# Optimization experiments

Measured on AMD Instinct MI355X. Metric: run time of the kernel, lower is better.

The kernel has to match this reference:

```python
import jax, jax.numpy as jnp
import numpy as np

D_MODEL = 1024
N_HEADS = 16
D_K = D_MODEL // N_HEADS
THETA = 10000.0
NEG_INF = -1e30


def _rope_tables(token_positions, d_k, theta=THETA):
    # freqs[t, i] = t / theta**(2i/d_k), i in [0, d_k/2)
    exponent = jnp.arange(0, d_k, 2, dtype=jnp.float32)  # [d_k/2]
    inv_freq = 1.0 / theta ** (exponent / d_k)
    freqs = token_positions.astype(jnp.float32)[:, None] * inv_freq[None, :]  # [s, d_k/2]
    return jnp.cos(freqs), jnp.sin(freqs)


def _apply_rope(x, cos, sin):
    # x: [..., s, d_k]; interleaved pair rotation (pairs are (x[2i], x[2i+1]))
    x1 = x[..., 0::2]
    x2 = x[..., 1::2]
    r1 = x1 * cos - x2 * sin
    r2 = x1 * sin + x2 * cos
    return jnp.stack([r1, r2], axis=-1).reshape(x.shape)


def setup_inputs() -> dict:
    key = jax.random.key(0)
    ks = jax.random.split(key, 5)
    b, s = 2, 2048
    scale = np.sqrt(2.0 / (D_MODEL + D_MODEL))
    return {
        "x": jax.random.normal(ks[0], (b, s, D_MODEL), dtype=jnp.float32),
        "Wq": jax.random.normal(ks[1], (D_MODEL, D_MODEL), dtype=jnp.float32) * scale,
        "Wk": jax.random.normal(ks[2], (D_MODEL, D_MODEL), dtype=jnp.float32) * scale,
        "Wv": jax.random.normal(ks[3], (D_MODEL, D_MODEL), dtype=jnp.float32) * scale,
        "Wo": jax.random.normal(ks[4], (D_MODEL, D_MODEL), dtype=jnp.float32) * scale,
        "token_positions": jnp.arange(s, dtype=jnp.int64 if jax.config.jax_enable_x64 else jnp.int32),
    }


def reference(x, Wq, Wk, Wv, Wo, token_positions):
    b, s, _ = x.shape
    # QKV projections: weight stored [in, out]
    q = jnp.einsum('bsi,io->bso', x, Wq)
    k = jnp.einsum('bsi,io->bso', x, Wk)
    v = jnp.einsum('bsi,io->bso', x, Wv)
    # split heads: [b, h, s, d_k]
    q = q.reshape(b, s, N_HEADS, D_K).transpose(0, 2, 1, 3)
    k = k.reshape(b, s, N_HEADS, D_K).transpose(0, 2, 1, 3)
    v = v.reshape(b, s, N_HEADS, D_K).transpose(0, 2, 1, 3)
    # RoPE
    cos, sin = _rope_tables(token_positions, D_K)
    q = _apply_rope(q, cos, sin)
    k = _apply_rope(k, cos, sin)
    # causal attention with full materialized scores (faithful to source)
    scores = jnp.einsum('bhid,bhjd->bhij', q, k) / jnp.sqrt(jnp.float32(D_K))
    mask = jnp.tril(jnp.ones((s, s), dtype=bool))
    scores = jnp.where(mask, scores, NEG_INF)
    probs = jax.nn.softmax(scores, axis=-1)
    out = jnp.einsum('bhij,bhjd->bhid', probs, v)
    out = out.transpose(0, 2, 1, 3).reshape(b, s, D_MODEL)
    return jnp.einsum('bsi,io->bso', out, Wo)
```

## Files before the change

kernel.cpp:

```cpp
#include <hip/hip_runtime.h>
#include <hip/hip_bf16.h>
#include <cmath>

#define S_LEN 2048
#define DMODEL 1024
#define NHEADS 16
#define DK 64
#define BATCH 2
#define MTOT (BATCH * S_LEN)

using short8 = __attribute__((ext_vector_type(8))) short;
using floatx4 = __attribute__((ext_vector_type(4))) float;

__device__ __forceinline__ unsigned short f2b(float f) {
    union { float f; unsigned u; } v; v.f = f;
    unsigned r = v.u + 0x7fff + ((v.u >> 16) & 1);
    return (unsigned short)(r >> 16);
}

__device__ __forceinline__ unsigned pack2(float a, float b) {
    float2 t; t.x = a; t.y = b;
    __hip_bfloat162 h = __float22bfloat162_rn(t);
    union { __hip_bfloat162 h; unsigned u; } v; v.h = h;
    return v.u;
}

__device__ __forceinline__ void gload16(const void* g, void* l) {
    __builtin_amdgcn_global_load_lds(
        (const __attribute__((address_space(1))) unsigned int*)g,
        (__attribute__((address_space(3))) unsigned int*)l, 16, 0, 0);
}

#define FENCE() asm volatile("" ::: "memory")

__global__ __launch_bounds__(256) void prep_k(
    const float* __restrict__ x, unsigned short* __restrict__ xb,
    const int* __restrict__ tokpos, float* __restrict__ ct, float* __restrict__ st,
    const float* W0, const float* W1, const float* W2, const float* W3,
    unsigned short* T0, unsigned short* T1, unsigned short* T2, unsigned short* T3) {
    __shared__ float t[64][65];
    const int b = blockIdx.x;
    if (b < 2048) {
        int i = (b * 256 + threadIdx.x) * 8;
        float4 a = *(const float4*)(x + i);
        float4 bb = *(const float4*)(x + i + 4);
        short8 o;
        o[0] = f2b(a.x); o[1] = f2b(a.y); o[2] = f2b(a.z); o[3] = f2b(a.w);
        o[4] = f2b(bb.x); o[5] = f2b(bb.y); o[6] = f2b(bb.z); o[7] = f2b(bb.w);
        *(short8*)(xb + i) = o;
    } else if (b < 2304) {
        int idx = (b - 2048) * 256 + threadIdx.x;
        int si = idx >> 5;
        int ip = idx & 31;
        float pos = (float)tokpos[si];
        float inv_freq = powf(10000.0f, -(float)(2 * ip) / 64.0f);
        float ang = pos * inv_freq;
        ct[idx] = cosf(ang);
        st[idx] = sinf(ang);
    } else {
        int id = b - 2304;
        int z = id >> 8;
        int bx = id & 15, by = (id >> 4) & 15;
        const float* W = z == 0 ? W0 : z == 1 ? W1 : z == 2 ? W2 : W3;
        unsigned short* T = z == 0 ? T0 : z == 1 ? T1 : z == 2 ? T2 : T3;
        const bool perm = (z < 2);
        int n0 = bx * 64, k0 = by * 64;
        int rr = threadIdx.x >> 6, cc = threadIdx.x & 63;
#pragma unroll
        for (int r = 0; r < 16; r++) {
            int row = r * 4 + rr;
            t[row][cc] = W[(size_t)(k0 + row) * DMODEL + n0 + cc];
        }
        __syncthreads();
#pragma unroll
        for (int r = 0; r < 16; r++) {
            int row = r * 4 + rr;
            int drow = perm ? (((row & 1) ? 32 : 0) + (row >> 1)) : row;
            T[(size_t)(n0 + drow) * DMODEL + k0 + cc] = f2b(t[cc][row]);
        }
    }
}

__global__ __launch_bounds__(256) void vtrans_k(const unsigned short* __restrict__ V,
                                                unsigned short* __restrict__ Vt) {
    __shared__ unsigned short t[64][72];
    const int tid = threadIdx.x;
    const int s0 = blockIdx.x * 64, d0 = blockIdx.y * 64;
    const int bb = s0 >> 11;
#pragma unroll
    for (int it = 0; it < 4; it++) {
        int e = (it * 256 + tid) * 4;
        int r = e >> 6, c = e & 63;
        *(ushort4*)&t[r][c] = *(const ushort4*)(V + (size_t)(s0 + r) * DMODEL + d0 + c);
    }
    __syncthreads();
#pragma unroll
    for (int it = 0; it < 4; it++) {
        int e = (it * 256 + tid) * 4;
        int r = e >> 6, c = e & 63;
        ushort4 v;
        v.x = t[c + 0][r]; v.y = t[c + 1][r];
        v.z = t[c + 2][r]; v.w = t[c + 3][r];
        *(ushort4*)(Vt + (size_t)(bb * 1024 + d0 + r) * S_LEN + (s0 & (S_LEN - 1)) + c) = v;
    }
}

__global__ __launch_bounds__(512, 2) void mm_k(
    const unsigned short* __restrict__ A,
    const unsigned short* __restrict__ Bt0, const unsigned short* __restrict__ Bt1,
    const unsigned short* __restrict__ Bt2,
    void* C0, void* C1, void* C2,
    const float* __restrict__ ct, const float* __restrict__ st, int kind) {
    __shared__ __align__(16) unsigned short blob[10 * 8192];

    const int z = blockIdx.z;
    const unsigned short* Bt = z == 0 ? Bt0 : z == 1 ? Bt1 : Bt2;
    void* C = z == 0 ? C0 : z == 1 ? C1 : C2;
    const int mode = (kind == 1) ? 0 : (z == 2 ? 3 : 1);
    const float qscale = (z == 0 && kind == 0) ? 0.18033688011112042f : 1.0f;

    const int tid = threadIdx.x;
    const int w = tid >> 6, lane = tid & 63;
    const int l15 = lane & 15, quad = lane >> 4;
    const int wr = w >> 2, wc = w & 3;
    const int m0 = blockIdx.x * 256, n0 = blockIdx.y * 256;

    const int rbase = (w >> 1) * 16 + l15;
    const int cbase = (w & 1) * 32 + quad * 8;

    floatx4 acc[8][4];
#pragma unroll
    for (int i = 0; i < 8; i++)
#pragma unroll
        for (int j = 0; j < 4; j++) acc[i][j] = (floatx4){0.f, 0.f, 0.f, 0.f};

    auto stage_half = [&](int h) {
        const int ts = h >> 2, part = h & 3;
        const int slot = h % 10;
        const unsigned short* src =
            (part < 2 ? A + (((size_t)(m0 + part * 128 + rbase)) << 10)
                      : Bt + (((size_t)(n0 + (part - 2) * 128 + rbase)) << 10))
            + (size_t)ts * 64 + cbase;
        char* d = (char*)blob + slot * 16384 + w * 1024;
        gload16(src, d);
        gload16(src + (64 << 10), d + 8192);
    };

#pragma unroll
    for (int h = 0; h < 6; ++h) stage_half(h);
    asm volatile("s_waitcnt vmcnt(4)" ::: "memory");
    FENCE(); __builtin_amdgcn_s_barrier(); FENCE();

    short8 af[4][2];
    for (int t = 0; t < 16; ++t) {
        const int sb = (4 * t) % 10;
        int sA = sb + wr;            if (sA >= 10) sA -= 10;
        int sB = sb + 2 + (wc >> 1); if (sB >= 10) sB -= 10;
        const char* LA = (const char*)blob + sA * 16384;
        const char* LB = (const char*)blob + sB * 16384;
#pragma unroll
        for (int q = 0; q < 4; ++q) {
            const int rh = q >> 1, ch = q & 1;
            if (ch == 0) {
#pragma unroll
                for (int ii = 0; ii < 4; ++ii)
#pragma unroll
                    for (int kh = 0; kh < 2; ++kh)
                        af[ii][kh] = *(const short8*)(LA + ((rh * 4 + ii) * 2 + kh) * 1024 + lane * 16);
            }
            short8 bf[2][2];
#pragma unroll
            for (int jj = 0; jj < 2; ++jj)
#pragma unroll
                for (int kh = 0; kh < 2; ++kh)
                    bf[jj][kh] = *(const short8*)(LB + (((wc & 1) * 4 + ch * 2 + jj) * 2 + kh) * 1024 + lane * 16);
            const int h = 4 * t + q + 6;
            if (h < 64) stage_half(h);
            if (q == 3) {
                if (t == 14) asm volatile("s_waitcnt vmcnt(0)" ::: "memory");
                else         asm volatile("s_waitcnt vmcnt(4)" ::: "memory");
            }
            FENCE(); __builtin_amdgcn_s_barrier(); FENCE();
            __builtin_amdgcn_s_setprio(1);
#pragma unroll
            for (int ii = 0; ii < 4; ++ii)
#pragma unroll
                for (int jj = 0; jj < 2; ++jj) {
                    floatx4 a0 = acc[rh * 4 + ii][ch * 2 + jj];
                    a0 = __builtin_amdgcn_mfma_f32_16x16x32_bf16(af[ii][0], bf[jj][0], a0, 0, 0, 0);
                    a0 = __builtin_amdgcn_mfma_f32_16x16x32_bf16(af[ii][1], bf[jj][1], a0, 0, 0, 0);
                    acc[rh * 4 + ii][ch * 2 + jj] = a0;
                }
            __builtin_amdgcn_s_setprio(0);
            FENCE(); __builtin_amdgcn_s_barrier(); FENCE();
        }
    }

#pragma unroll
    for (int i = 0; i < 8; i++) {
        const int rowb = m0 + wr * 128 + i * 16 + quad * 4;
        if (mode == 0) {
            float* Cf = (float*)C;
#pragma unroll
            for (int j = 0; j < 4; j++) {
                int colb = n0 + wc * 64 + j * 16 + l15;
#pragma unroll
                for (int r = 0; r < 4; r++)
                    Cf[(size_t)(rowb + r) * DMODEL + colb] = acc[i][j][r];
            }
        } else if (mode == 1) {
            unsigned short* Cb = (unsigned short*)C;
#pragma unroll
            for (int jh = 0; jh < 2; jh++) {
                int ip = jh * 16 + l15;
                int cole = n0 + wc * 64 + jh * 16 + l15;
#pragma unroll
                for (int r = 0; r < 4; r++) {
                    int row = rowb + r;
                    int si = row & (S_LEN - 1);
                    float c = ct[si * 32 + ip] * qscale;
                    float s = st[si * 32 + ip] * qscale;
                    float e = acc[i][jh][r];
                    float od = acc[i][jh + 2][r];
                    Cb[(size_t)row * DMODEL + cole] = f2b(e * c - od * s);
                    Cb[(size_t)row * DMODEL + cole + 32] = f2b(e * s + od * c);
                }
            }
        } else {
            unsigned short* Cb = (unsigned short*)C;
#pragma unroll
            for (int j = 0; j < 4; j++) {
                int colb = n0 + wc * 64 + j * 16 + l15;
#pragma unroll
                for (int r = 0; r < 4; r++)
                    Cb[(size_t)(rowb + r) * DMODEL + colb] = f2b(acc[i][j][r]);
            }
        }
    }
}

__global__ __launch_bounds__(512) void attn_k(const unsigned short* __restrict__ Q,
                                              const unsigned short* __restrict__ K,
                                              const unsigned short* __restrict__ Vt,
                                              unsigned short* __restrict__ O) {
    __shared__ __align__(16) unsigned short Kblob[2][4096];
    __shared__ __align__(16) unsigned short Vblob[2][4096];
    __shared__ __align__(16) unsigned short Ps[8][16 * 72];

    const int tid = threadIdx.x;
    const int w = tid >> 6, lane = tid & 63;
    const int l15 = lane & 15, quad = lane >> 4;
    const int idx = blockIdx.x;
    const int qt = 15 - (idx >> 5);
    const int bh = idx & 31;
    const int bb = bh >> 4, h = bh & 15;
    const int qbase = qt * 128 + w * 16;
    const int qrow = qbase + l15;

    const size_t qoff = (size_t)(bb * S_LEN + qbase + l15) * DMODEL + h * DK;
    short8 aq0 = *(const short8*)(Q + qoff + quad * 8);
    short8 aq1 = *(const short8*)(Q + qoff + 32 + quad * 8);

    floatx4 o[4];
#pragma unroll
    for (int f = 0; f < 4; f++) o[f] = (floatx4){0.f, 0.f, 0.f, 0.f};
    float mv = -1e30f, lv = 0.f;

    const unsigned short* Kb = K + (size_t)(bb * S_LEN) * DMODEL + h * DK;
    const unsigned short* Vb = Vt + (size_t)(bb * 1024 + h * DK) * S_LEN;
    unsigned short* ps = &Ps[w][0];

    auto stage = [&](int b, int kb) {
#pragma unroll
        for (int it = 0; it < 2; it++) {
            int g = it * 8 + w;
            if (g < 8) {
                const unsigned short* gp =
                    Kb + (size_t)(kb + (g >> 1) * 16 + l15) * DMODEL + (g & 1) * 32 + quad * 8;
                gload16(gp, (char*)&Kblob[b][0] + g * 1024);
            } else {
                int gv = g - 8;
                const unsigned short* gp =
                    Vb + (size_t)((gv >> 1) * 16 + l15) * S_LEN + kb + (gv & 1) * 32 + quad * 8;
                gload16(gp, (char*)&Vblob[b][0] + gv * 1024);
            }
        }
    };

    const int nkt = 2 * qt + 2;
    stage(0, 0);
    for (int kt = 0; kt < nkt; kt++) {
        const int b = kt & 1;
        const int kb = kt * 64;
        __syncthreads();
        if (kt + 1 < nkt) stage(b ^ 1, (kt + 1) * 64);

        const unsigned short* kbb = &Kblob[b][0];
        floatx4 c[4];
#pragma unroll
        for (int g = 0; g < 4; g++) {
            short8 kf0 = *(const short8*)(kbb + (g * 2 + 0) * 512 + lane * 8);
            short8 kf1 = *(const short8*)(kbb + (g * 2 + 1) * 512 + lane * 8);
            floatx4 t = {0.f, 0.f, 0.f, 0.f};
            t = __builtin_amdgcn_mfma_f32_16x16x32_bf16(kf0, aq0, t, 0, 0, 0);
            c[g] = __builtin_amdgcn_mfma_f32_16x16x32_bf16(kf1, aq1, t, 0, 0, 0);
        }

        float sv[16];
        if (kb + 63 <= qbase) {
#pragma unroll
            for (int g = 0; g < 4; g++)
#pragma unroll
                for (int r = 0; r < 4; r++) sv[g * 4 + r] = c[g][r];
        } else {
#pragma unroll
            for (int g = 0; g < 4; g++)
#pragma unroll
                for (int r = 0; r < 4; r++) {
                    int key = kb + g * 16 + quad * 4 + r;
                    sv[g * 4 + r] = (key <= qrow) ? c[g][r] : -1e30f;
                }
        }
        float mx = sv[0];
#pragma unroll
        for (int i = 1; i < 16; i++) mx = fmaxf(mx, sv[i]);
        mx = fmaxf(mx, __shfl_xor(mx, 16));
        mx = fmaxf(mx, __shfl_xor(mx, 32));
        float mnew = fmaxf(mv, mx);
        float alpha = exp2f(mv - mnew);
        mv = mnew;
        float p[16], psum = 0.f;
#pragma unroll
        for (int i = 0; i < 16; i++) {
            p[i] = exp2f(sv[i] - mnew);
            psum += p[i];
        }
        lv = lv * alpha + psum;

#pragma unroll
        for (int g = 0; g < 4; g++) {
            uint2 pk;
            pk.x = pack2(p[g * 4 + 0], p[g * 4 + 1]);
            pk.y = pack2(p[g * 4 + 2], p[g * 4 + 3]);
            *(uint2*)(ps + l15 * 72 + g * 16 + quad * 4) = pk;
        }
#pragma unroll
        for (int f = 0; f < 4; f++) {
            o[f][0] *= alpha; o[f][1] *= alpha;
            o[f][2] *= alpha; o[f][3] *= alpha;
        }
        short8 pf0 = *(const short8*)(ps + l15 * 72 + quad * 8);
        short8 pf1 = *(const short8*)(ps + l15 * 72 + 32 + quad * 8);
        const unsigned short* vbb = &Vblob[b][0];
#pragma unroll
        for (int f = 0; f < 4; f++) {
            short8 vf0 = *(const short8*)(vbb + (f * 2 + 0) * 512 + lane * 8);
            short8 vf1 = *(const short8*)(vbb + (f * 2 + 1) * 512 + lane * 8);
            o[f] = __builtin_amdgcn_mfma_f32_16x16x32_bf16(vf0, pf0, o[f], 0, 0, 0);
            o[f] = __builtin_amdgcn_mfma_f32_16x16x32_bf16(vf1, pf1, o[f], 0, 0, 0);
        }
    }

    lv += __shfl_xor(lv, 16);
    lv += __shfl_xor(lv, 32);
    float inv = 1.0f / lv;
    __syncthreads();
#pragma unroll
    for (int f = 0; f < 4; f++) {
        uint2 pk;
        pk.x = pack2(o[f][0] * inv, o[f][1] * inv);
        pk.y = pack2(o[f][2] * inv, o[f][3] * inv);
        *(uint2*)(ps + l15 * 72 + f * 16 + quad * 4) = pk;
    }
    short8 r0 = *(const short8*)(ps + l15 * 72 + quad * 8);
    short8 r1 = *(const short8*)(ps + l15 * 72 + 32 + quad * 8);
    size_t obase = (size_t)(bb * S_LEN + qbase + l15) * DMODEL + h * DK;
    *(short8*)(O + obase + quad * 8) = r0;
    *(short8*)(O + obase + 32 + quad * 8) = r1;
}

extern "C" void kernel_launch(void* const* d_in, const int* in_sizes, int n_in,
                              void* d_out, int out_size, void* d_ws,
                              size_t ws_size, hipStream_t stream) {
    const float* x = (const float*)d_in[0];
    const float* Wq = (const float*)d_in[1];
    const float* Wk = (const float*)d_in[2];
    const float* Wv = (const float*)d_in[3];
    const float* Wo = (const float*)d_in[4];
    const int* tokpos = (const int*)d_in[5];
    float* out = (float*)d_out;

    const size_t MD = (size_t)MTOT * DMODEL;
    const size_t WD = (size_t)DMODEL * DMODEL;
    unsigned short* xb = (unsigned short*)d_ws;
    unsigned short* Wqt = xb + MD;
    unsigned short* Wkt = Wqt + WD;
    unsigned short* Wvt = Wkt + WD;
    unsigned short* Wot = Wvt + WD;
    unsigned short* Q = Wot + WD;
    unsigned short* K = Q + MD;
    unsigned short* V = K + MD;
    unsigned short* Vt = V + MD;
    float* ct = (float*)(Vt + MD);
    float* st = ct + S_LEN * 32;
    unsigned short* O = V;

    prep_k<<<dim3(3328), dim3(256), 0, stream>>>(x, xb, tokpos, ct, st,
                                                 Wq, Wk, Wv, Wo, Wqt, Wkt, Wvt, Wot);

    mm_k<<<dim3(16, 4, 3), dim3(512), 0, stream>>>(xb, Wqt, Wkt, Wvt,
                                                   (void*)Q, (void*)K, (void*)V, ct, st, 0);
    vtrans_k<<<dim3(64, 16), dim3(256), 0, stream>>>(V, Vt);
    attn_k<<<dim3(512), dim3(512), 0, stream>>>(Q, K, Vt, O);
    mm_k<<<dim3(16, 4, 1), dim3(512), 0, stream>>>(O, Wot, Wot, Wot,
                                                   (void*)out, (void*)out, (void*)out, ct, st, 1);
}
```

Baseline: 214.9 us.

## Triple-buffer K/V staging with explicit waitcnt barriers and skip masked tiles

Replaces the double-buffered K/V staging with a three-slot ring that prefetches two tiles ahead, using explicit vmcnt waits and raw s_barrier instead of __syncthreads. Each wave now loads one K and one V chunk per stage through incrementing pointers, and waves skip the compute for key tiles fully above their causal diagonal. It also adds a lazy rescale that only updates the running max when it actually grows, raises MFMA priority with setprio, sets a min-blocks launch bound, and changes block ordering for part of the grid. Extra LDS for the third buffer may reduce occupancy, and the hand-written wait counts depend on the gload16 instruction count.

```diff
diff --git a/kernel.cpp b/kernel.cpp
--- a/kernel.cpp
+++ b/kernel.cpp
@@ -239,19 +239,19 @@
     }
 }
 
-__global__ __launch_bounds__(512) void attn_k(const unsigned short* __restrict__ Q,
-                                              const unsigned short* __restrict__ K,
-                                              const unsigned short* __restrict__ Vt,
-                                              unsigned short* __restrict__ O) {
-    __shared__ __align__(16) unsigned short Kblob[2][4096];
-    __shared__ __align__(16) unsigned short Vblob[2][4096];
+__global__ __launch_bounds__(512, 4) void attn_k(const unsigned short* __restrict__ Q,
+                                                 const unsigned short* __restrict__ K,
+                                                 const unsigned short* __restrict__ Vt,
+                                                 unsigned short* __restrict__ O) {
+    __shared__ __align__(16) unsigned short Kblob[3][4096];
+    __shared__ __align__(16) unsigned short Vblob[3][4096];
     __shared__ __align__(16) unsigned short Ps[8][16 * 72];
 
     const int tid = threadIdx.x;
     const int w = tid >> 6, lane = tid & 63;
     const int l15 = lane & 15, quad = lane >> 4;
     const int idx = blockIdx.x;
-    const int qt = 15 - (idx >> 5);
+    const int qt = (idx < 256) ? 15 - (idx >> 5) : ((idx - 256) >> 5);
     const int bh = idx & 31;
     const int bb = bh >> 4, h = bh & 15;
     const int qbase = qt * 128 + w * 16;
@@ -270,95 +270,111 @@
     const unsigned short* Vb = Vt + (size_t)(bb * 1024 + h * DK) * S_LEN;
     unsigned short* ps = &Ps[w][0];
 
-    auto stage = [&](int b, int kb) {
-#pragma unroll
-        for (int it = 0; it < 2; it++) {
-            int g = it * 8 + w;
-            if (g < 8) {
-                const unsigned short* gp =
-                    Kb + (size_t)(kb + (g >> 1) * 16 + l15) * DMODEL + (g & 1) * 32 + quad * 8;
-                gload16(gp, (char*)&Kblob[b][0] + g * 1024);
+    const unsigned short* kp = Kb + (size_t)((w >> 1) * 16 + l15) * DMODEL + (w & 1) * 32 + quad * 8;
+    const unsigned short* vp = Vb + (size_t)((w >> 1) * 16 + l15) * S_LEN + (w & 1) * 32 + quad * 8;
+
+    auto stage = [&](int slot) {
+        gload16(kp, (char*)&Kblob[slot][0] + w * 1024);
+        gload16(vp, (char*)&Vblob[slot][0] + w * 1024);
+        kp += 64 * DMODEL;
+        vp += 64;
+    };
+
+    const int nkt = 2 * qt + 2;
+    stage(0); stage(1);
+    asm volatile("s_waitcnt vmcnt(2)" ::: "memory");
+    FENCE(); __builtin_amdgcn_s_barrier(); FENCE();
+
+    int sl = 0, s2 = 2;
+    for (int kt = 0; kt < nkt; kt++) {
+        if (kt + 2 < nkt) stage(s2);
+
+        if (kt * 64 <= qbase + 15) {
+            const int kb = kt * 64;
+            const unsigned short* kbb = &Kblob[sl][0];
+            floatx4 c[4];
+            __builtin_amdgcn_s_setprio(1);
+#pragma unroll
+            for (int g = 0; g < 4; g++) {
+                short8 kf0 = *(const short8*)(kbb + (g * 2 + 0) * 512 + lane * 8);
+                short8 kf1 = *(const short8*)(kbb + (g * 2 + 1) * 512 + lane * 8);
+                floatx4 t = {0.f, 0.f, 0.f, 0.f};
+                t = __builtin_amdgcn_mfma_f32_16x16x32_bf16(kf0, aq0, t, 0, 0, 0);
+                c[g] = __builtin_amdgcn_mfma_f32_16x16x32_bf16(kf1, aq1, t, 0, 0, 0);
+            }
+            __builtin_amdgcn_s_setprio(0);
+
+            float sv[16];
+            if (kb + 63 <= qbase) {
+#pragma unroll
+                for (int g = 0; g < 4; g++)
+#pragma unroll
+                    for (int r = 0; r < 4; r++) sv[g * 4 + r] = c[g][r];
             } else {
-                int gv = g - 8;
-                const unsigned short* gp =
-                    Vb + (size_t)((gv >> 1) * 16 + l15) * S_LEN + kb + (gv & 1) * 32 + quad * 8;
-                gload16(gp, (char*)&Vblob[b][0] + gv * 1024);
-            }
-        }
-    };
-
-    const int nkt = 2 * qt + 2;
-    stage(0, 0);
-    for (int kt = 0; kt < nkt; kt++) {
-        const int b = kt & 1;
-        const int kb = kt * 64;
-        __syncthreads();
-        if (kt + 1 < nkt) stage(b ^ 1, (kt + 1) * 64);
-
-        const unsigned short* kbb = &Kblob[b][0];
-        floatx4 c[4];
-#pragma unroll
-        for (int g = 0; g < 4; g++) {
-            short8 kf0 = *(const short8*)(kbb + (g * 2 + 0) * 512 + lane * 8);
-            short8 kf1 = *(const short8*)(kbb + (g * 2 + 1) * 512 + lane * 8);
-            floatx4 t = {0.f, 0.f, 0.f, 0.f};
-            t = __builtin_amdgcn_mfma_f32_16x16x32_bf16(kf0, aq0, t, 0, 0, 0);
-            c[g] = __builtin_amdgcn_mfma_f32_16x16x32_bf16(kf1, aq1, t, 0, 0, 0);
-        }
-
-        float sv[16];
-        if (kb + 63 <= qbase) {
-#pragma unroll
-            for (int g = 0; g < 4; g++)
-#pragma unroll
-                for (int r = 0; r < 4; r++) sv[g * 4 + r] = c[g][r];
-        } else {
-#pragma unroll
-            for (int g = 0; g < 4; g++)
-#pragma unroll
-                for (int r = 0; r < 4; r++) {
-                    int key = kb + g * 16 + quad * 4 + r;
-                    sv[g * 4 + r] = (key <= qrow) ? c[g][r] : -1e30f;
+#pragma unroll
+                for (int g = 0; g < 4; g++)
+#pragma unroll
+                    for (int r = 0; r < 4; r++) {
+                        int key = kb + g * 16 + quad * 4 + r;
+                        sv[g * 4 + r] = (key <= qrow) ? c[g][r] : -1e30f;
+                    }
+            }
+            float m0 = fmaxf(fmaxf(sv[0], sv[1]), sv[2]);
+            float m1 = fmaxf(fmaxf(sv[3], sv[4]), sv[5]);
+            float m2 = fmaxf(fmaxf(sv[6], sv[7]), sv[8]);
+            float m3 = fmaxf(fmaxf(sv[9], sv[10]), sv[11]);
+            float m4 = fmaxf(fmaxf(sv[12], sv[13]), sv[14]);
+            float mx = fmaxf(fmaxf(fmaxf(m0, m1), fmaxf(m2, m3)), fmaxf(m4, sv[15]));
+            mx = fmaxf(mx, __shfl_xor(mx, 16));
+            mx = fmaxf(mx, __shfl_xor(mx, 32));
+
+            if (!__all(mx <= mv)) {
+                float mnew = fmaxf(mv, mx);
+                float alpha = exp2f(mv - mnew);
+                mv = mnew;
+                lv *= alpha;
+#pragma unroll
+                for (int f = 0; f < 4; f++) {
+                    o[f][0] *= alpha; o[f][1] *= alpha;
+                    o[f][2] *= alpha; o[f][3] *= alpha;
                 }
-        }
-        float mx = sv[0];
-#pragma unroll
-        for (int i = 1; i < 16; i++) mx = fmaxf(mx, sv[i]);
-        mx = fmaxf(mx, __shfl_xor(mx, 16));
-        mx = fmaxf(mx, __shfl_xor(mx, 32));
-        float mnew = fmaxf(mv, mx);
-        float alpha = exp2f(mv - mnew);
-        mv = mnew;
-        float p[16], psum = 0.f;
-#pragma unroll
-        for (int i = 0; i < 16; i++) {
-            p[i] = exp2f(sv[i] - mnew);
-            psum += p[i];
-        }
-        lv = lv * alpha + psum;
-
-#pragma unroll
-        for (int g = 0; g < 4; g++) {
-            uint2 pk;
-            pk.x = pack2(p[g * 4 + 0], p[g * 4 + 1]);
-            pk.y = pack2(p[g * 4 + 2], p[g * 4 + 3]);
-            *(uint2*)(ps + l15 * 72 + g * 16 + quad * 4) = pk;
-        }
-#pragma unroll
-        for (int f = 0; f < 4; f++) {
-            o[f][0] *= alpha; o[f][1] *= alpha;
-            o[f][2] *= alpha; o[f][3] *= alpha;
-        }
-        short8 pf0 = *(const short8*)(ps + l15 * 72 + quad * 8);
-        short8 pf1 = *(const short8*)(ps + l15 * 72 + 32 + quad * 8);
-        const unsigned short* vbb = &Vblob[b][0];
-#pragma unroll
-        for (int f = 0; f < 4; f++) {
-            short8 vf0 = *(const short8*)(vbb + (f * 2 + 0) * 512 + lane * 8);
-            short8 vf1 = *(const short8*)(vbb + (f * 2 + 1) * 512 + lane * 8);
-            o[f] = __builtin_amdgcn_mfma_f32_16x16x32_bf16(vf0, pf0, o[f], 0, 0, 0);
-            o[f] = __builtin_amdgcn_mfma_f32_16x16x32_bf16(vf1, pf1, o[f], 0, 0, 0);
-        }
+            }
+            float p[16], psum = 0.f;
+#pragma unroll
+            for (int i = 0; i < 16; i++) {
+                p[i] = exp2f(sv[i] - mv);
+                psum += p[i];
+            }
+            lv += psum;
+
+#pragma unroll
+            for (int g = 0; g < 4; g++) {
+                uint2 pk;
+                pk.x = pack2(p[g * 4 + 0], p[g * 4 + 1]);
+                pk.y = pack2(p[g * 4 + 2], p[g * 4 + 3]);
+                *(uint2*)(ps + l15 * 72 + g * 16 + quad * 4) = pk;
+            }
+            short8 pf0 = *(const short8*)(ps + l15 * 72 + quad * 8);
+            short8 pf1 = *(const short8*)(ps + l15 * 72 + 32 + quad * 8);
+            const unsigned short* vbb = &Vblob[sl][0];
+            __builtin_amdgcn_s_setprio(1);
+#pragma unroll
+            for (int f = 0; f < 4; f++) {
+                short8 vf0 = *(const short8*)(vbb + (f * 2 + 0) * 512 + lane * 8);
+                short8 vf1 = *(const short8*)(vbb + (f * 2 + 1) * 512 + lane * 8);
+                o[f] = __builtin_amdgcn_mfma_f32_16x16x32_bf16(vf0, pf0, o[f], 0, 0, 0);
+                o[f] = __builtin_amdgcn_mfma_f32_16x16x32_bf16(vf1, pf1, o[f], 0, 0, 0);
+            }
+            __builtin_amdgcn_s_setprio(0);
+        }
+
+        if (kt + 1 < nkt) {
+            if (kt + 2 < nkt) asm volatile("s_waitcnt vmcnt(2)" ::: "memory");
+            else              asm volatile("s_waitcnt vmcnt(0)" ::: "memory");
+            FENCE(); __builtin_amdgcn_s_barrier(); FENCE();
+        }
+        sl = (sl == 2) ? 0 : sl + 1;
+        s2 = (s2 == 2) ? 0 : s2 + 1;
     }
 
     lv += __shfl_xor(lv, 16);
```

New measurement: 226.4 us. 1.05x slower.
